# Optimization experiments

Measured on AMD Instinct MI355X. Metric: run time of the kernel, lower is better.

The kernel has to match this reference:

```python
import jax, jax.numpy as jnp
import numpy as np

EPS = 1e-6
EVAL_STEPS = 7
INV_T = 1.0
B, C, H, W = 16, 512, 64, 64
S, R = 1, 64


def setup_inputs() -> dict:
    key = jax.random.key(0)
    kx, kb = jax.random.split(key)
    x = jax.random.uniform(kx, (B, C, H, W), dtype=jnp.float32)
    # bases: F.normalize(rand(S, D, R), dim=1), repeated over batch -> [B*S, D, R]
    D = C // S
    b = jax.random.uniform(kb, (S, D, R), dtype=jnp.float32)
    b = b / jnp.clip(jnp.linalg.norm(b, axis=1, keepdims=True), 1e-12)
    bases = jnp.tile(b, (B, 1, 1))  # [B*S, D, R]
    return {"x": x, "bases": bases}


def _local_step(x, bases, coef):
    # x: [BS, D, N], bases: [BS, D, R], coef: [BS, N, R]
    numer = jnp.einsum('bdn,bdr->bnr', x, bases)
    denom = jnp.einsum('bnr,brk->bnk', coef, jnp.einsum('bdr,bdk->brk', bases, bases))
    coef = coef * numer / (denom + EPS)
    numer = jnp.einsum('bdn,bnr->bdr', x, coef)
    denom = jnp.einsum('bdr,brk->bdk', bases, jnp.einsum('bnr,bnk->brk', coef, coef))
    bases = bases * numer / (denom + EPS)
    return bases, coef


def reference(x, bases):
    batch, channels, height, width = x.shape
    scale = channels // S
    xf = x.reshape(batch * S, scale, height * width)  # [BS, D, N]
    # local_inference (eval mode: eval_steps iterations)
    coef = jnp.einsum('bdn,bdr->bnr', xf, bases)
    coef = jax.nn.softmax(INV_T * coef, axis=-1)
    for _ in range(EVAL_STEPS):
        bases, coef = _local_step(xf, bases, coef)
    # compute_coef: one extra coef update
    numer = jnp.einsum('bdn,bdr->bnr', xf, bases)
    denom = jnp.einsum('bnr,brk->bnk', coef, jnp.einsum('bdr,bdk->brk', bases, bases))
    coef = coef * numer / (denom + EPS)
    out = jnp.einsum('bdr,bnr->bdn', bases, coef)  # bases @ coef^T
    return out.reshape(batch, channels, height, width)
```

## Files before the change

kernel.cpp:

```cpp
#include <hip/hip_runtime.h>
#include <math.h>

#define EPS 1e-6f

constexpr int BSZ = 16;
constexpr int DD  = 512;
constexpr int NN  = 4096;
constexpr int RR  = 64;
constexpr int STEPS = 7;
constexpr int NS_B  = 8;
constexpr int NS_C  = 32;
constexpr int NS_N2 = 8;

typedef _Float16 half_t;
typedef __attribute__((ext_vector_type(8))) _Float16 half8;
typedef __attribute__((ext_vector_type(4))) float f32x4;

__device__ __forceinline__ void fma4s(float4& a, const float4& b, float s) {
  a.x = fmaf(b.x, s, a.x); a.y = fmaf(b.y, s, a.y);
  a.z = fmaf(b.z, s, a.z); a.w = fmaf(b.w, s, a.w);
}
__device__ __forceinline__ void add4(float4& a, const float4& b) {
  a.x += b.x; a.y += b.y; a.z += b.z; a.w += b.w;
}
__device__ __forceinline__ f32x4 mfmah(half8 a, half8 b, f32x4 c) {
  return __builtin_amdgcn_mfma_f32_16x16x32_f16(a, b, c, 0, 0, 0);
}

__device__ __forceinline__ void gload16(const float* g, float* l) {
  __builtin_amdgcn_global_load_lds(
      (const __attribute__((address_space(1))) void*)g,
      (__attribute__((address_space(3))) void*)l, 16, 0, 0);
}

__global__ void __launch_bounds__(256) tcvt16_kernel(const float* __restrict__ src,
                                                     half_t* __restrict__ dh,
                                                     int R, int C) {
  __shared__ float tileT[64 * 65];
  const int b = blockIdx.z, c0 = blockIdx.x << 6, r0 = blockIdx.y << 6;
  const float* sp = src + (long long)b * R * C;
  const int t = threadIdx.x;
  #pragma unroll
  for (int i = 0; i < 4; ++i) {
    const int idx = t + (i << 8);
    const int row = idx >> 4, c4 = (idx & 15) << 2;
    const float4 v = *(const float4*)&sp[(long long)(r0 + row) * C + c0 + c4];
    tileT[(c4 + 0) * 65 + row] = v.x;
    tileT[(c4 + 1) * 65 + row] = v.y;
    tileT[(c4 + 2) * 65 + row] = v.z;
    tileT[(c4 + 3) * 65 + row] = v.w;
  }
  __syncthreads();
  const int orow = t >> 2, och = (t & 3) << 4;
  half8 h0, h1;
  #pragma unroll
  for (int j = 0; j < 8; ++j) h0[j] = (half_t)tileT[orow * 65 + och + j];
  #pragma unroll
  for (int j = 0; j < 8; ++j) h1[j] = (half_t)tileT[orow * 65 + och + 8 + j];
  const long long ob = ((long long)b * C + c0 + orow) * R + r0 + och;
  *(half8*)&dh[ob] = h0;
  *(half8*)&dh[ob + 8] = h1;
}

__global__ void __launch_bounds__(256) cast16_kernel(const float* __restrict__ src,
                                                     half_t* __restrict__ dst,
                                                     long long n) {
  const long long i = ((long long)blockIdx.x * 256 + threadIdx.x) * 8;
  if (i >= n) return;
  const float4 a = *(const float4*)&src[i];
  const float4 c = *(const float4*)&src[i + 4];
  half8 h;
  h[0] = (half_t)a.x; h[1] = (half_t)a.y; h[2] = (half_t)a.z; h[3] = (half_t)a.w;
  h[4] = (half_t)c.x; h[5] = (half_t)c.y; h[6] = (half_t)c.z; h[7] = (half_t)c.w;
  *(half8*)&dst[i] = h;
}

__global__ void __launch_bounds__(256) btb16_kernel(const half_t* __restrict__ BT,
                                                    half_t* __restrict__ Gh) {
  __shared__ float red[64 * 64];
  const int b = blockIdx.x;
  const int t = threadIdx.x;
  const int w = t >> 6;
  const int l = t & 63;
  const int row16 = l & 15;
  const int koff  = (l >> 4) << 3;

  const half_t* ap = BT + ((long long)b * RR + row16) * DD + (w << 7) + koff;

  f32x4 acc[4][4];
  #pragma unroll
  for (int i = 0; i < 4; ++i)
    #pragma unroll
    for (int j = 0; j < 4; ++j) acc[i][j] = (f32x4){0.f, 0.f, 0.f, 0.f};

  #pragma unroll
  for (int kt = 0; kt < 4; ++kt) {
    const int ko = kt << 5;
    half8 af[4];
    #pragma unroll
    for (int rs = 0; rs < 4; ++rs) af[rs] = *(const half8*)&ap[(long long)rs * 16 * DD + ko];
    #pragma unroll
    for (int r1 = 0; r1 < 4; ++r1)
      #pragma unroll
      for (int r2 = 0; r2 < 4; ++r2)
        acc[r1][r2] = mfmah(af[r1], af[r2], acc[r1][r2]);
  }
  for (int ww = 0; ww < 4; ++ww) {
    if (w == ww) {
      #pragma unroll
      for (int r1 = 0; r1 < 4; ++r1)
        #pragma unroll
        for (int r2 = 0; r2 < 4; ++r2)
          #pragma unroll
          for (int j = 0; j < 4; ++j) {
            const int row = (r1 << 4) + ((l >> 4) << 2) + j;
            const int col = (r2 << 4) + row16;
            if (ww == 0) red[row * 64 + col] = acc[r1][r2][j];
            else         red[row * 64 + col] += acc[r1][r2][j];
          }
    }
    __syncthreads();
  }
  for (int i = t; i < 512; i += 256) {
    half8 h;
    #pragma unroll
    for (int j = 0; j < 8; ++j) h[j] = (half_t)red[(i << 3) + j];
    *(half8*)&Gh[(long long)b * 4096 + (i << 3)] = h;
  }
}

template <int MODE>
__global__ void __launch_bounds__(128) fused16_kernel(const half_t* __restrict__ xT,
                                                      const half_t* __restrict__ BT,
                                                      const half_t* __restrict__ Gh,
                                                      float* __restrict__ coef,
                                                      half_t* __restrict__ cbT,
                                                      half_t* __restrict__ cN) {
  __shared__ half_t ctile[(MODE == 1) ? 64 * 40 : 8];
  const int b  = blockIdx.y;
  const int n0 = blockIdx.x << 5;
  const int t  = threadIdx.x;
  const int w  = t >> 6;
  const int l  = t & 63;
  const int row16 = l & 15;
  const int koff  = (l >> 4) << 3;
  const int nrb   = n0 + (w << 4);

  const half_t* ap = xT + ((long long)b * NN + nrb + row16) * DD + koff;
  const half_t* bp = BT + ((long long)b * RR + row16) * DD + koff;

  f32x4 acc[4];
  #pragma unroll
  for (int rs = 0; rs < 4; ++rs) acc[rs] = (f32x4){0.f, 0.f, 0.f, 0.f};

  #pragma unroll
  for (int kt = 0; kt < 16; ++kt) {
    const int ko = kt << 5;
    const half8 av = *(const half8*)&ap[ko];
    #pragma unroll
    for (int rs = 0; rs < 4; ++rs) {
      const half8 bv = *(const half8*)&bp[rs * 16 * DD + ko];
      acc[rs] = mfmah(av, bv, acc[rs]);
    }
  }

  if constexpr (MODE == 0) {
    #pragma unroll
    for (int j = 0; j < 4; ++j) {
      float m = fmaxf(fmaxf(acc[0][j], acc[1][j]), fmaxf(acc[2][j], acc[3][j]));
      m = fmaxf(m, __shfl_xor(m, 1));
      m = fmaxf(m, __shfl_xor(m, 2));
      m = fmaxf(m, __shfl_xor(m, 4));
      m = fmaxf(m, __shfl_xor(m, 8));
      float s = 0.f;
      #pragma unroll
      for (int rs = 0; rs < 4; ++rs) { acc[rs][j] = __expf(acc[rs][j] - m); s += acc[rs][j]; }
      s += __shfl_xor(s, 1); s += __shfl_xor(s, 2);
      s += __shfl_xor(s, 4); s += __shfl_xor(s, 8);
      const float inv = 1.f / s;
      #pragma unroll
      for (int rs = 0; rs < 4; ++rs) acc[rs][j] *= inv;
    }
    #pragma unroll
    for (int rs = 0; rs < 4; ++rs)
      #pragma unroll
      for (int j = 0; j < 4; ++j)
        coef[((long long)b * NN + nrb + ((l >> 4) << 2) + j) * RR + (rs << 4) + row16] = acc[rs][j];
  } else {
    const float* crow = coef + ((long long)b * NN + nrb + row16) * RR;
    const half_t* ghb = Gh + (long long)b * 4096;
    f32x4 dn[4];
    #pragma unroll
    for (int rs = 0; rs < 4; ++rs) dn[rs] = (f32x4){0.f, 0.f, 0.f, 0.f};
    #pragma unroll
    for (int kt = 0; kt < 2; ++kt) {
      const int ko = (kt << 5) + koff;
      const float4 c0 = *(const float4*)&crow[ko];
      const float4 c1 = *(const float4*)&crow[ko + 4];
      half8 ch;
      ch[0] = (half_t)c0.x; ch[1] = (half_t)c0.y; ch[2] = (half_t)c0.z; ch[3] = (half_t)c0.w;
      ch[4] = (half_t)c1.x; ch[5] = (half_t)c1.y; ch[6] = (half_t)c1.z; ch[7] = (half_t)c1.w;
      #pragma unroll
      for (int rs = 0; rs < 4; ++rs) {
        const half8 gh = *(const half8*)&ghb[((rs << 4) + row16) * 64 + ko];
        dn[rs] = mfmah(ch, gh, dn[rs]);
      }
    }
    #pragma unroll
    for (int rs = 0; rs < 4; ++rs)
      #pragma unroll
      for (int j = 0; j < 4; ++j) {
        const int r = (rs << 4) + row16;
        const int nl = ((w << 4) + ((l >> 4) << 2) + j);
        const long long idx = ((long long)b * NN + n0 + nl) * RR + r;
        const float co = coef[idx];
        const float v  = co * acc[rs][j] / (dn[rs][j] + EPS);
        if constexpr (MODE == 1) {
          coef[idx] = v;
          ctile[r * 40 + nl] = (half_t)v;
        } else {
          cN[idx] = (half_t)v;
        }
      }
    if constexpr (MODE == 1) {
      __syncthreads();
      if (t < 64) {
        half_t* dst = cbT + ((long long)b * RR + t) * NN + n0;
        *(half8*)&dst[0]  = *(const half8*)&ctile[t * 40 + 0];
        *(half8*)&dst[8]  = *(const half8*)&ctile[t * 40 + 8];
        *(half8*)&dst[16] = *(const half8*)&ctile[t * 40 + 16];
        *(half8*)&dst[24] = *(const half8*)&ctile[t * 40 + 24];
      }
    }
  }
}

__global__ void __launch_bounds__(128) numer2ctc16_kernel(const half_t* __restrict__ xh,
                                                          const half_t* __restrict__ cbT,
                                                          float* __restrict__ n2p,
                                                          float* __restrict__ ctcp) {
  __shared__ float red[4096];
  const int b = blockIdx.z;
  const int s = blockIdx.y;
  const int t = threadIdx.x;
  const int w = t >> 6;
  const int l = t & 63;
  const int row16 = l & 15;
  const int koff  = (l >> 4) << 3;
  const int nbeg  = s * (NN / NS_N2);

  if (blockIdx.x == DD / 64) {
    const half_t* ap = cbT + ((long long)b * RR + row16) * NN + nbeg + (w << 8) + koff;
    f32x4 acc[4][4];
    #pragma unroll
    for (int i = 0; i < 4; ++i)
      #pragma unroll
      for (int j = 0; j < 4; ++j) acc[i][j] = (f32x4){0.f, 0.f, 0.f, 0.f};
    #pragma unroll
    for (int kt = 0; kt < 8; ++kt) {
      const int ko = kt << 5;
      half8 af[4];
      #pragma unroll
      for (int rs = 0; rs < 4; ++rs) af[rs] = *(const half8*)&ap[(long long)rs * 16 * NN + ko];
      #pragma unroll
      for (int r1 = 0; r1 < 4; ++r1)
        #pragma unroll
        for (int r2 = 0; r2 < 4; ++r2)
          acc[r1][r2] = mfmah(af[r1], af[r2], acc[r1][r2]);
    }
    if (w == 0) {
      #pragma unroll
      for (int r1 = 0; r1 < 4; ++r1)
        #pragma unroll
        for (int r2 = 0; r2 < 4; ++r2)
          #pragma unroll
          for (int j = 0; j < 4; ++j)
            red[((r1 << 4) + ((l >> 4) << 2) + j) * 64 + (r2 << 4) + row16] = acc[r1][r2][j];
    }
    __syncthreads();
    if (w == 1) {
      #pragma unroll
      for (int r1 = 0; r1 < 4; ++r1)
        #pragma unroll
        for (int r2 = 0; r2 < 4; ++r2)
          #pragma unroll
          for (int j = 0; j < 4; ++j)
            red[((r1 << 4) + ((l >> 4) << 2) + j) * 64 + (r2 << 4) + row16] += acc[r1][r2][j];
    }
    __syncthreads();
    float* op = ctcp + ((long long)s * BSZ + b) * 4096;
    for (int i = t; i < 1024; i += 128) ((float4*)op)[i] = ((const float4*)red)[i];
    return;
  }

  const int d0 = blockIdx.x << 6;
  const half_t* ap = xh + ((long long)b * DD + d0 + w * 32 + row16) * NN + nbeg + koff;
  const half_t* cp = cbT + ((long long)b * RR + row16) * NN + nbeg + koff;

  f32x4 acc[2][4];
  #pragma unroll
  for (int ds = 0; ds < 2; ++ds)
    #pragma unroll
    for (int rs = 0; rs < 4; ++rs) acc[ds][rs] = (f32x4){0.f, 0.f, 0.f, 0.f};

  #pragma unroll
  for (int kt = 0; kt < 16; ++kt) {
    const int ko = kt << 5;
    half8 av[2], bf[4];
    #pragma unroll
    for (int ds = 0; ds < 2; ++ds) av[ds] = *(const half8*)&ap[(long long)ds * 16 * NN + ko];
    #pragma unroll
    for (int rs = 0; rs < 4; ++rs) bf[rs] = *(const half8*)&cp[(long long)rs * 16 * NN + ko];
    #pragma unroll
    for (int ds = 0; ds < 2; ++ds)
      #pragma unroll
      for (int rs = 0; rs < 4; ++rs)
        acc[ds][rs] = mfmah(av[ds], bf[rs], acc[ds][rs]);
  }
  float* op = n2p + (((long long)s * BSZ + b) * DD + d0 + w * 32) * RR;
  #pragma unroll
  for (int ds = 0; ds < 2; ++ds)
    #pragma unroll
    for (int rs = 0; rs < 4; ++rs)
      #pragma unroll
      for (int j = 0; j < 4; ++j)
        op[(long long)(ds * 16 + ((l >> 4) << 2) + j) * RR + (rs << 4) + row16] = acc[ds][rs][j];
}

__global__ void __launch_bounds__(256) bupdate16_kernel(float* __restrict__ Bw,
                                                        const float* __restrict__ n2p,
                                                        const float* __restrict__ ctcp,
                                                        half_t* __restrict__ BbT,
                                                        half_t* __restrict__ bD) {
  __shared__ float ct[4096];
  const int b  = blockIdx.y;
  const int d0 = blockIdx.x << 6;
  const int t  = threadIdx.x;
  #pragma unroll
  for (int i = 0; i < 4; ++i) {
    const int w = t + (i << 8);
    float4 s4 = make_float4(0.f, 0.f, 0.f, 0.f);
    #pragma unroll
    for (int sp = 0; sp < NS_N2; ++sp)
      add4(s4, ((const float4*)(ctcp + ((long long)sp * BSZ + b) * 4096))[w]);
    ((float4*)ct)[w] = s4;
  }
  __syncthreads();
  const int dl = t >> 2;
  const int d  = d0 + dl;
  const int rq = (t & 3) << 4;

  float4 ns[4];
  #pragma unroll
  for (int j = 0; j < 4; ++j) ns[j] = make_float4(0.f, 0.f, 0.f, 0.f);
  for (int s = 0; s < NS_N2; ++s) {
    const float4* p = (const float4*)&n2p[(((long long)s * BSZ + b) * DD + d) * RR + rq];
    #pragma unroll
    for (int j = 0; j < 4; ++j) add4(ns[j], p[j]);
  }
  const float4* brow = (const float4*)&Bw[((long long)b * DD + d) * RR];
  float4 dn[4];
  #pragma unroll
  for (int j = 0; j < 4; ++j) dn[j] = make_float4(0.f, 0.f, 0.f, 0.f);
  for (int q = 0; q < 16; ++q) {
    const float4 b4 = brow[q];
    const float4* c0 = (const float4*)&ct[(4 * q + 0) * 64 + rq];
    const float4* c1 = (const float4*)&ct[(4 * q + 1) * 64 + rq];
    const float4* c2 = (const float4*)&ct[(4 * q + 2) * 64 + rq];
    const float4* c3 = (const float4*)&ct[(4 * q + 3) * 64 + rq];
    #pragma unroll
    for (int j = 0; j < 4; ++j) {
      fma4s(dn[j], c0[j], b4.x); fma4s(dn[j], c1[j], b4.y);
      fma4s(dn[j], c2[j], b4.z); fma4s(dn[j], c3[j], b4.w);
    }
  }
  float4* bp = (float4*)&Bw[((long long)b * DD + d) * RR + rq];
  float4 bo[4];
  #pragma unroll
  for (int j = 0; j < 4; ++j) bo[j] = bp[j];
  __syncthreads();
  half_t* tile = (half_t*)ct;
  float4 ov[4];
  #pragma unroll
  for (int j = 0; j < 4; ++j) {
    ov[j].x = bo[j].x * ns[j].x / (dn[j].x + EPS);
    ov[j].y = bo[j].y * ns[j].y / (dn[j].y + EPS);
    ov[j].z = bo[j].z * ns[j].z / (dn[j].z + EPS);
    ov[j].w = bo[j].w * ns[j].w / (dn[j].w + EPS);
    bp[j] = ov[j];
    tile[(rq + (j << 2) + 0) * 64 + dl] = (half_t)ov[j].x;
    tile[(rq + (j << 2) + 1) * 64 + dl] = (half_t)ov[j].y;
    tile[(rq + (j << 2) + 2) * 64 + dl] = (half_t)ov[j].z;
    tile[(rq + (j << 2) + 3) * 64 + dl] = (half_t)ov[j].w;
  }
  if (bD) {
    half_t* dst = bD + ((long long)b * DD + d) * RR + rq;
    half8 h0, h1;
    #pragma unroll
    for (int e = 0; e < 4; ++e) {
      h0[e] = (half_t)ov[0].x, h0[e] = h0[e];
    }
    h0[0] = (half_t)ov[0].x; h0[1] = (half_t)ov[0].y; h0[2] = (half_t)ov[0].z; h0[3] = (half_t)ov[0].w;
    h0[4] = (half_t)ov[1].x; h0[5] = (half_t)ov[1].y; h0[6] = (half_t)ov[1].z; h0[7] = (half_t)ov[1].w;
    h1[0] = (half_t)ov[2].x; h1[1] = (half_t)ov[2].y; h1[2] = (half_t)ov[2].z; h1[3] = (half_t)ov[2].w;
    h1[4] = (half_t)ov[3].x; h1[5] = (half_t)ov[3].y; h1[6] = (half_t)ov[3].z; h1[7] = (half_t)ov[3].w;
    *(half8*)&dst[0] = h0;
    *(half8*)&dst[8] = h1;
  }
  __syncthreads();
  const int r = t >> 2, qc = t & 3;
  half_t* dstT = BbT + ((long long)b * RR + r) * DD + d0 + (qc << 4);
  *(half8*)&dstT[0] = *(const half8*)&tile[r * 64 + (qc << 4)];
  *(half8*)&dstT[8] = *(const half8*)&tile[r * 64 + (qc << 4) + 8];
}

__global__ void __launch_bounds__(256) out16_kernel(const half_t* __restrict__ bD,
                                                    const half_t* __restrict__ cN,
                                                    float* __restrict__ out) {
  __shared__ float ot[16 * 264];
  const int n0 = blockIdx.x << 8;
  const int d0 = blockIdx.y << 4;
  const int b  = blockIdx.z;
  const int t  = threadIdx.x;
  const int w  = t >> 6;
  const int l  = t & 63;
  const int row16 = l & 15;
  const int koff  = (l >> 4) << 3;

  const half_t* ap = bD + ((long long)b * DD + d0 + row16) * RR + koff;
  const half_t* bp = cN + ((long long)b * NN + n0 + (w << 6) + row16) * RR + koff;

  f32x4 acc[4];
  #pragma unroll
  for (int ns = 0; ns < 4; ++ns) acc[ns] = (f32x4){0.f, 0.f, 0.f, 0.f};

  #pragma unroll
  for (int kt = 0; kt < 2; ++kt) {
    const int ko = kt << 5;
    const half8 av = *(const half8*)&ap[ko];
    #pragma unroll
    for (int ns = 0; ns < 4; ++ns) {
      const half8 bv = *(const half8*)&bp[(long long)ns * 16 * RR + ko];
      acc[ns] = mfmah(av, bv, acc[ns]);
    }
  }
  #pragma unroll
  for (int ns = 0; ns < 4; ++ns)
    #pragma unroll
    for (int j = 0; j < 4; ++j)
      ot[(((l >> 4) << 2) + j) * 264 + (w << 6) + (ns << 4) + row16] = acc[ns][j];
  __syncthreads();
  #pragma unroll
  for (int k = 0; k < 4; ++k) {
    const int idx = t + (k << 8);
    const int row = idx >> 6, c4 = (idx & 63) << 2;
    const float4 v = *(const float4*)&ot[row * 264 + c4];
    *(float4*)&out[((long long)b * DD + d0 + row) * NN + n0 + c4] = v;
  }
}


__global__ void __launch_bounds__(256) gram_kernel(const float* __restrict__ M,
                                                   float* __restrict__ outp,
                                                   int rowsPerWave,
                                                   long long batchStride) {
  __shared__ float red[RR * RR];
  const int lane = threadIdx.x & 63;
  const int wid  = threadIdx.x >> 6;
  const int b    = blockIdx.y;
  const long long rowbase = (long long)(blockIdx.x * 4 + wid) * rowsPerWave;
  const float* Mp = M + (long long)b * batchStride + rowbase * RR;
  float acc[RR];
  #pragma unroll
  for (int k = 0; k < RR; ++k) acc[k] = 0.f;
  #pragma unroll 2
  for (int rr = 0; rr < rowsPerWave; ++rr) {
    const float v = Mp[(long long)rr * RR + lane];
    #pragma unroll
    for (int k = 0; k < RR; ++k) acc[k] = fmaf(__shfl(v, k), v, acc[k]);
  }
  for (int w = 0; w < 4; ++w) {
    if (wid == w) {
      if (w == 0) {
        #pragma unroll
        for (int k = 0; k < RR; ++k) red[k * RR + lane] = acc[k];
      } else {
        #pragma unroll
        for (int k = 0; k < RR; ++k) red[k * RR + lane] += acc[k];
      }
    }
    __syncthreads();
  }
  float* op = outp + ((long long)blockIdx.x * BSZ + b) * (RR * RR);
  for (int i = threadIdx.x; i < RR * RR; i += 256) op[i] = red[i];
}

template <int MODE>
__global__ void __launch_bounds__(128) fused_coef_kernel(const float* __restrict__ X,
                                                         const float* __restrict__ Bw,
                                                         const float* __restrict__ btbp,
                                                         float* __restrict__ coef) {
  __shared__ float lds[8192];
  const int b    = blockIdx.y;
  const int n0   = blockIdx.x << 6;
  const int t    = threadIdx.x;
  const int wid  = t >> 6;
  const int lane = t & 63;
  const int rgrp = t & 7;
  const int ngrp = t >> 3;
  const int nl   = ngrp << 2;
  const int r0   = rgrp << 3;
  const float* Xp = X  + (long long)b * DD * NN + n0;
  const float* Bp = Bw + (long long)b * DD * RR;

  float4 acc[4][2];
  #pragma unroll
  for (int i = 0; i < 4; ++i) { acc[i][0] = make_float4(0,0,0,0); acc[i][1] = make_float4(0,0,0,0); }

  auto stage = [&](int buf, int d0) {
    float* xd = lds + (buf << 11);
    float* bd = lds + 4096 + (buf << 11);
    const int rsub = lane >> 4;
    const int c4   = (lane & 15) << 2;
    #pragma unroll
    for (int j = 0; j < 4; ++j) {
      const int q   = (wid << 2) + j;
      const int row = (q << 2) + rsub;
      gload16(&Xp[(long long)(d0 + row) * NN + c4], xd + (q << 8));
      gload16(&Bp[(long long)(d0 + row) * RR + c4], bd + (q << 8));
    }
  };

  stage(0, 0);
  __syncthreads();
  for (int kt = 0; kt < 16; ++kt) {
    const int cur = kt & 1;
    if (kt + 1 < 16) stage(cur ^ 1, (kt + 1) << 5);
    const float* xs = lds + (cur << 11);
    const float* bs = lds + 4096 + (cur << 11);
    #pragma unroll 8
    for (int dd = 0; dd < 32; ++dd) {
      const float4 xv  = *(const float4*)&xs[(dd << 6) + nl];
      const float4 bv0 = *(const float4*)&bs[(dd << 6) + r0];
      const float4 bv1 = *(const float4*)&bs[(dd << 6) + r0 + 4];
      fma4s(acc[0][0], bv0, xv.x); fma4s(acc[0][1], bv1, xv.x);
      fma4s(acc[1][0], bv0, xv.y); fma4s(acc[1][1], bv1, xv.y);
      fma4s(acc[2][0], bv0, xv.z); fma4s(acc[2][1], bv1, xv.z);
      fma4s(acc[3][0], bv0, xv.w); fma4s(acc[3][1], bv1, xv.w);
    }
    __syncthreads();
  }

  if constexpr (MODE == 0) {
    #pragma unroll
    for (int i = 0; i < 4; ++i) {
      float4 a0 = acc[i][0], a1 = acc[i][1];
      float m = fmaxf(fmaxf(fmaxf(a0.x, a0.y), fmaxf(a0.z, a0.w)),
                      fmaxf(fmaxf(a1.x, a1.y), fmaxf(a1.z, a1.w)));
      m = fmaxf(m, __shfl_xor(m, 1));
      m = fmaxf(m, __shfl_xor(m, 2));
      m = fmaxf(m, __shfl_xor(m, 4));
      a0.x = __expf(a0.x - m); a0.y = __expf(a0.y - m);
      a0.z = __expf(a0.z - m); a0.w = __expf(a0.w - m);
      a1.x = __expf(a1.x - m); a1.y = __expf(a1.y - m);
      a1.z = __expf(a1.z - m); a1.w = __expf(a1.w - m);
      float s = a0.x + a0.y + a0.z + a0.w + a1.x + a1.y + a1.z + a1.w;
      s += __shfl_xor(s, 1); s += __shfl_xor(s, 2); s += __shfl_xor(s, 4);
      const float inv = 1.f / s;
      a0.x *= inv; a0.y *= inv; a0.z *= inv; a0.w *= inv;
      a1.x *= inv; a1.y *= inv; a1.z *= inv; a1.w *= inv;
      float* cp = coef + ((long long)b * NN + n0 + nl + i) * RR + r0;
      *(float4*)&cp[0] = a0;
      *(float4*)&cp[4] = a1;
    }
  } else {
    float4* G4  = (float4*)lds;
    float4* CO4 = (float4*)(lds + 4096);
    #pragma unroll
    for (int j = 0; j < 8; ++j) {
      const int wi = t + (j << 7);
      float4 ssum = make_float4(0,0,0,0);
      #pragma unroll
      for (int sp = 0; sp < NS_B; ++sp)
        add4(ssum, ((const float4*)(btbp + ((long long)sp * BSZ + b) * 4096))[wi]);
      G4[wi] = ssum;
    }
    const float4* cof4 = (const float4*)(coef + ((long long)b * NN + n0) * RR);
    #pragma unroll
    for (int j = 0; j < 8; ++j) {
      const int wi = t + (j << 7);
      const int row = wi >> 4, c4 = wi & 15;
      CO4[(row << 4) + (c4 ^ ((row >> 2) & 7))] = cof4[wi];
    }
    __syncthreads();
    const int g = ngrp & 7;
    float4 dn[4][2];
    #pragma unroll
    for (int i = 0; i < 4; ++i) { dn[i][0] = make_float4(0,0,0,0); dn[i][1] = make_float4(0,0,0,0); }
    #pragma unroll 4
    for (int kq = 0; kq < 16; ++kq) {
      float4 g0[4], g1[4];
      #pragma unroll
      for (int jj = 0; jj < 4; ++jj) {
        g0[jj] = G4[(((kq << 2) + jj) << 4) + (rgrp << 1)];
        g1[jj] = G4[(((kq << 2) + jj) << 4) + (rgrp << 1) + 1];
      }
      #pragma unroll
      for (int i = 0; i < 4; ++i) {
        const float4 cv = CO4[((nl + i) << 4) + (kq ^ g)];
        fma4s(dn[i][0], g0[0], cv.x); fma4s(dn[i][1], g1[0], cv.x);
        fma4s(dn[i][0], g0[1], cv.y); fma4s(dn[i][1], g1[1], cv.y);
        fma4s(dn[i][0], g0[2], cv.z); fma4s(dn[i][1], g1[2], cv.z);
        fma4s(dn[i][0], g0[3], cv.w); fma4s(dn[i][1], g1[3], cv.w);
      }
    }
    #pragma unroll
    for (int i = 0; i < 4; ++i) {
      const int row = nl + i;
      const float4 c0 = CO4[(row << 4) + ((rgrp << 1) ^ g)];
      const float4 c1 = CO4[(row << 4) + (((rgrp << 1) + 1) ^ g)];
      float4 o0, o1;
      o0.x = c0.x * acc[i][0].x / (dn[i][0].x + EPS);
      o0.y = c0.y * acc[i][0].y / (dn[i][0].y + EPS);
      o0.z = c0.z * acc[i][0].z / (dn[i][0].z + EPS);
      o0.w = c0.w * acc[i][0].w / (dn[i][0].w + EPS);
      o1.x = c1.x * acc[i][1].x / (dn[i][1].x + EPS);
      o1.y = c1.y * acc[i][1].y / (dn[i][1].y + EPS);
      o1.z = c1.z * acc[i][1].z / (dn[i][1].z + EPS);
      o1.w = c1.w * acc[i][1].w / (dn[i][1].w + EPS);
      float* cp = coef + ((long long)b * NN + n0 + row) * RR + r0;
      *(float4*)&cp[0] = o0;
      *(float4*)&cp[4] = o1;
    }
  }
}

__global__ void __launch_bounds__(128) numer2_kernel(const float* __restrict__ X,
                                                     const float* __restrict__ coef,
                                                     float* __restrict__ n2p) {
  __shared__ float lds[8192];
  const int b    = blockIdx.z;
  const int s    = blockIdx.y;
  const int d0   = blockIdx.x << 6;
  const int t    = threadIdx.x;
  const int wid  = t >> 6;
  const int lane = t & 63;
  const int rgrp = t & 7;
  const int dgrp = t >> 3;
  const int dl   = dgrp << 2;
  const int r0   = rgrp << 3;
  const int nbeg = s * (NN / NS_N2);
  const float* Xp = X + (long long)b * DD * NN + (long long)d0 * NN;
  const float* Cp = coef + (long long)b * NN * RR;

  float4 acc[4][2];
  #pragma unroll
  for (int i = 0; i < 4; ++i) { acc[i][0] = make_float4(0,0,0,0); acc[i][1] = make_float4(0,0,0,0); }

  auto stage = [&](int buf, int nb) {
    float* xd = lds + (buf << 11);
    float* cd = lds + 4096 + (buf << 11);
    {
      const int rsub = lane >> 3, c4 = lane & 7;
      #pragma unroll
      for (int j = 0; j < 4; ++j) {
        const int q   = (wid << 2) + j;
        const int row = (q << 3) + rsub;
        const int sc  = (c4 ^ ((row >> 2) & 7)) << 2;
        gload16(&Xp[(long long)row * NN + nb + sc], xd + (q << 8));
      }
    }
    {
      const int rsub = lane >> 4, c4 = (lane & 15) << 2;
      #pragma unroll
      for (int j = 0; j < 4; ++j) {
        const int q   = (wid << 2) + j;
        const int row = (q << 2) + rsub;
        gload16(&Cp[(long long)(nb + row) * RR + c4], cd + (q << 8));
      }
    }
  };

  stage(0, nbeg);
  __syncthreads();
  const int g = dgrp & 7;
  for (int kt = 0; kt < (NN / NS_N2) / 32; ++kt) {
    const int cur = kt & 1;
    if (kt + 1 < (NN / NS_N2) / 32) stage(cur ^ 1, nbeg + ((kt + 1) << 5));
    const float* xs = lds + (cur << 11);
    const float* cs = lds + 4096 + (cur << 11);
    #pragma unroll 8
    for (int nn = 0; nn < 32; ++nn) {
      const int col = ((((nn >> 2) ^ g) << 2) + (nn & 3));
      float xe[4];
      #pragma unroll
      for (int i = 0; i < 4; ++i) xe[i] = xs[((dl + i) << 5) + col];
      const float4 cv0 = *(const float4*)&cs[(nn << 6) + r0];
      const float4 cv1 = *(const float4*)&cs[(nn << 6) + r0 + 4];
      #pragma unroll
      for (int i = 0; i < 4; ++i) {
        fma4s(acc[i][0], cv0, xe[i]);
        fma4s(acc[i][1], cv1, xe[i]);
      }
    }
    __syncthreads();
  }
  #pragma unroll
  for (int i = 0; i < 4; ++i) {
    float* op = n2p + (((long long)s * BSZ + b) * DD + d0 + dl + i) * RR + r0;
    *(float4*)&op[0] = acc[i][0];
    *(float4*)&op[4] = acc[i][1];
  }
}

__global__ void __launch_bounds__(256) bupdate_fb_kernel(float* __restrict__ Bw,
                                                         const float* __restrict__ n2p,
                                                         const float* __restrict__ ctcp,
                                                         int ns2) {
  __shared__ float ct[4096];
  const int b  = blockIdx.y;
  const int d0 = blockIdx.x << 6;
  #pragma unroll
  for (int i = 0; i < 4; ++i) {
    const int w = threadIdx.x + (i << 8);
    float4 s = make_float4(0.f, 0.f, 0.f, 0.f);
    for (int sp = 0; sp < NS_C; ++sp)
      add4(s, ((const float4*)(ctcp + ((long long)sp * BSZ + b) * 4096))[w]);
    ((float4*)ct)[w] = s;
  }
  __syncthreads();
  const int d  = d0 + (threadIdx.x >> 2);
  const int rq = (threadIdx.x & 3) << 4;

  float4 ns[4];
  #pragma unroll
  for (int j = 0; j < 4; ++j) ns[j] = make_float4(0.f, 0.f, 0.f, 0.f);
  for (int s = 0; s < ns2; ++s) {
    const float4* p = (const float4*)&n2p[(((long long)s * BSZ + b) * DD + d) * RR + rq];
    #pragma unroll
    for (int j = 0; j < 4; ++j) add4(ns[j], p[j]);
  }
  const float4* brow = (const float4*)&Bw[((long long)b * DD + d) * RR];
  float4 dn[4];
  #pragma unroll
  for (int j = 0; j < 4; ++j) dn[j] = make_float4(0.f, 0.f, 0.f, 0.f);
  for (int q = 0; q < 16; ++q) {
    const float4 b4 = brow[q];
    const float4* c0 = (const float4*)&ct[(4 * q + 0) * 64 + rq];
    const float4* c1 = (const float4*)&ct[(4 * q + 1) * 64 + rq];
    const float4* c2 = (const float4*)&ct[(4 * q + 2) * 64 + rq];
    const float4* c3 = (const float4*)&ct[(4 * q + 3) * 64 + rq];
    #pragma unroll
    for (int j = 0; j < 4; ++j) {
      fma4s(dn[j], c0[j], b4.x); fma4s(dn[j], c1[j], b4.y);
      fma4s(dn[j], c2[j], b4.z); fma4s(dn[j], c3[j], b4.w);
    }
  }
  float4* bp = (float4*)&Bw[((long long)b * DD + d) * RR + rq];
  float4 bo[4];
  #pragma unroll
  for (int j = 0; j < 4; ++j) bo[j] = bp[j];
  __syncthreads();
  #pragma unroll
  for (int j = 0; j < 4; ++j) {
    float4 o;
    o.x = bo[j].x * ns[j].x / (dn[j].x + EPS);
    o.y = bo[j].y * ns[j].y / (dn[j].y + EPS);
    o.z = bo[j].z * ns[j].z / (dn[j].z + EPS);
    o.w = bo[j].w * ns[j].w / (dn[j].w + EPS);
    bp[j] = o;
  }
}

__global__ void __launch_bounds__(256) out_kernel(const float* __restrict__ Bw,
                                                  const float* __restrict__ coef,
                                                  float* __restrict__ out) {
  __shared__ float bt [64 * 68];
  __shared__ float ctl[64 * 68];
  const int n0 = blockIdx.x << 6;
  const int d0 = blockIdx.y << 6;
  const int b  = blockIdx.z;
  const int tx = threadIdx.x & 15;
  const int ty = threadIdx.x >> 4;
  for (int t = threadIdx.x; t < 1024; t += 256) {
    const int row = t >> 4, c4 = (t & 15) << 2;
    const float4 v = *(const float4*)&Bw[((long long)b * DD + d0 + row) * RR + c4];
    bt[(c4 + 0) * 68 + row] = v.x; bt[(c4 + 1) * 68 + row] = v.y;
    bt[(c4 + 2) * 68 + row] = v.z; bt[(c4 + 3) * 68 + row] = v.w;
  }
  for (int t = threadIdx.x; t < 1024; t += 256) {
    const int row = t >> 4, c4 = (t & 15) << 2;
    const float4 v = *(const float4*)&coef[((long long)b * NN + n0 + row) * RR + c4];
    ctl[(c4 + 0) * 68 + row] = v.x; ctl[(c4 + 1) * 68 + row] = v.y;
    ctl[(c4 + 2) * 68 + row] = v.z; ctl[(c4 + 3) * 68 + row] = v.w;
  }
  __syncthreads();
  float4 ai[4];
  #pragma unroll
  for (int i = 0; i < 4; ++i) ai[i] = make_float4(0.f, 0.f, 0.f, 0.f);
  #pragma unroll 8
  for (int r = 0; r < 64; ++r) {
    const float4 bv = *(const float4*)&bt [r * 68 + (ty << 2)];
    const float4 cv = *(const float4*)&ctl[r * 68 + (tx << 2)];
    fma4s(ai[0], cv, bv.x); fma4s(ai[1], cv, bv.y);
    fma4s(ai[2], cv, bv.z); fma4s(ai[3], cv, bv.w);
  }
  #pragma unroll
  for (int i = 0; i < 4; ++i)
    *(float4*)&out[((long long)b * DD + d0 + (ty << 2) + i) * NN + n0 + (tx << 2)] = ai[i];
}

extern "C" void kernel_launch(void* const* d_in, const int* in_sizes, int n_in,
                              void* d_out, int out_size, void* d_ws, size_t ws_size,
                              hipStream_t stream) {
  const float* x        = (const float*)d_in[0];
  const float* bases_in = (const float*)d_in[1];
  float* out = (float*)d_out;
  float* ws  = (float*)d_ws;

  float* coef    = ws;
  float* bases_w = coef + (long long)BSZ * NN * RR;
  float* btbp    = bases_w + (long long)BSZ * DD * RR;
  float* ctcp    = btbp + (long long)NS_B * BSZ * 4096;
  float* n2p     = ctcp + (long long)NS_C * BSZ * 4096;
  float* ctcs    = n2p + (long long)NS_N2 * BSZ * DD * RR;
  half_t* xT16   = (half_t*)(ctcs + (long long)BSZ * 4096);
  half_t* xd16   = xT16 + (long long)BSZ * NN * DD;
  half_t* BbT16  = xd16 + (long long)BSZ * NN * DD;
  half_t* cbT16  = BbT16 + (long long)BSZ * RR * DD;
  half_t* Gh16   = cbT16 + (long long)BSZ * RR * NN;
  const long long need = (long long)((char*)(Gh16 + (long long)BSZ * 4096) - (char*)d_ws);

  half_t* cN16 = (half_t*)n2p;
  half_t* bD16 = (half_t*)btbp;

  const dim3 blk256(256);
  const dim3 blk128(128);

  hipMemcpyAsync(bases_w, bases_in, sizeof(float) * BSZ * DD * RR,
                 hipMemcpyDeviceToDevice, stream);

  if ((long long)ws_size >= need) {
    cast16_kernel<<<dim3(16384), blk256, 0, stream>>>(x, xd16, (long long)BSZ * DD * NN);
    tcvt16_kernel<<<dim3(NN / 64, DD / 64, BSZ), blk256, 0, stream>>>(x, xT16, DD, NN);
    tcvt16_kernel<<<dim3(1, DD / 64, BSZ), blk256, 0, stream>>>(bases_w, BbT16, DD, RR);
    fused16_kernel<0><<<dim3(NN / 32, BSZ), blk128, 0, stream>>>(
        xT16, BbT16, nullptr, coef, nullptr, nullptr);

    for (int it = 0; it < STEPS; ++it) {
      btb16_kernel<<<dim3(BSZ), blk256, 0, stream>>>(BbT16, Gh16);
      fused16_kernel<1><<<dim3(NN / 32, BSZ), blk128, 0, stream>>>(
          xT16, BbT16, Gh16, coef, cbT16, nullptr);
      numer2ctc16_kernel<<<dim3(DD / 64 + 1, NS_N2, BSZ), blk128, 0, stream>>>(
          xd16, cbT16, n2p, ctcp);
      bupdate16_kernel<<<dim3(DD / 64, BSZ), blk256, 0, stream>>>(
          bases_w, n2p, ctcp, BbT16, (it == STEPS - 1) ? bD16 : nullptr);
    }
    btb16_kernel<<<dim3(BSZ), blk256, 0, stream>>>(BbT16, Gh16);
    fused16_kernel<2><<<dim3(NN / 32, BSZ), blk128, 0, stream>>>(
        xT16, BbT16, Gh16, coef, nullptr, cN16);
    out16_kernel<<<dim3(NN / 256, DD / 16, BSZ), blk256, 0, stream>>>(bD16, cN16, out);
  } else {
    fused_coef_kernel<0><<<dim3(NN / 64, BSZ), blk128, 0, stream>>>(x, bases_w, nullptr, coef);
    for (int it = 0; it < STEPS; ++it) {
      gram_kernel<<<dim3(NS_B, BSZ), blk256, 0, stream>>>(bases_w, btbp, DD / (NS_B * 4),
                                                          (long long)DD * RR);
      fused_coef_kernel<1><<<dim3(NN / 64, BSZ), blk128, 0, stream>>>(x, bases_w, btbp, coef);
      gram_kernel<<<dim3(NS_C, BSZ), blk256, 0, stream>>>(coef, ctcp, NN / (NS_C * 4),
                                                          (long long)NN * RR);
      numer2_kernel<<<dim3(DD / 64, NS_N2, BSZ), blk128, 0, stream>>>(x, coef, n2p);
      bupdate_fb_kernel<<<dim3(DD / 64, BSZ), blk256, 0, stream>>>(bases_w, n2p, ctcp, NS_N2);
    }
    gram_kernel<<<dim3(NS_B, BSZ), blk256, 0, stream>>>(bases_w, btbp, DD / (NS_B * 4),
                                                        (long long)DD * RR);
    fused_coef_kernel<1><<<dim3(NN / 64, BSZ), blk128, 0, stream>>>(x, bases_w, btbp, coef);
    out_kernel<<<dim3(NN / 64, DD / 64, BSZ), blk256, 0, stream>>>(bases_w, coef, out);
  }
}
```

Baseline: 923.5 us.

## Fuse x conversions into one pass and fold bases Gram into bases update

Merges the two fp16 conversions of x (plain cast and transpose) into one kernel that reads x once and writes both layouts. Removes the per-iteration btb16 launch by computing each 64-row slice's partial B^T B inside bupdate16 with MFMA and atomically accumulating into an fp32 Gram buffer, which numer2ctc16 zeroes beforehand. The fused coefficient kernel now reads the fp32 Gram and converts it to half on the fly. This trades launches and one full pass over x for fp32 atomics and some extra fp32 loads.

New measurement: 880.7 us. 1.05x faster.

```diff
diff --git a/kernel.cpp b/kernel.cpp
--- a/kernel.cpp
+++ b/kernel.cpp
@@ -14,6 +14,7 @@
 
 typedef _Float16 half_t;
 typedef __attribute__((ext_vector_type(8))) _Float16 half8;
+typedef __attribute__((ext_vector_type(4))) _Float16 half4v;
 typedef __attribute__((ext_vector_type(4))) float f32x4;
 
 __device__ __forceinline__ void fma4s(float4& a, const float4& b, float s) {
@@ -31,6 +32,38 @@
   __builtin_amdgcn_global_load_lds(
       (const __attribute__((address_space(1))) void*)g,
       (__attribute__((address_space(3))) void*)l, 16, 0, 0);
+}
+
+__global__ void __launch_bounds__(256) xcvt16_kernel(const float* __restrict__ src,
+                                                     half_t* __restrict__ xd,
+                                                     half_t* __restrict__ xT) {
+  __shared__ float tileT[64 * 65];
+  const int b = blockIdx.z, c0 = blockIdx.x << 6, r0 = blockIdx.y << 6;
+  const float* sp = src + (long long)b * DD * NN;
+  const int t = threadIdx.x;
+  #pragma unroll
+  for (int i = 0; i < 4; ++i) {
+    const int idx = t + (i << 8);
+    const int row = idx >> 4, c4 = (idx & 15) << 2;
+    const float4 v = *(const float4*)&sp[(long long)(r0 + row) * NN + c0 + c4];
+    half4v h;
+    h[0] = (half_t)v.x; h[1] = (half_t)v.y; h[2] = (half_t)v.z; h[3] = (half_t)v.w;
+    *(half4v*)&xd[((long long)b * DD + r0 + row) * NN + c0 + c4] = h;
+    tileT[(c4 + 0) * 65 + row] = v.x;
+    tileT[(c4 + 1) * 65 + row] = v.y;
+    tileT[(c4 + 2) * 65 + row] = v.z;
+    tileT[(c4 + 3) * 65 + row] = v.w;
+  }
+  __syncthreads();
+  const int orow = t >> 2, och = (t & 3) << 4;
+  half8 h0, h1;
+  #pragma unroll
+  for (int j = 0; j < 8; ++j) h0[j] = (half_t)tileT[orow * 65 + och + j];
+  #pragma unroll
+  for (int j = 0; j < 8; ++j) h1[j] = (half_t)tileT[orow * 65 + och + 8 + j];
+  const long long ob = ((long long)b * NN + c0 + orow) * DD + r0 + och;
+  *(half8*)&xT[ob] = h0;
+  *(half8*)&xT[ob + 8] = h1;
 }
 
 __global__ void __launch_bounds__(256) tcvt16_kernel(const float* __restrict__ src,
@@ -62,21 +95,8 @@
   *(half8*)&dh[ob + 8] = h1;
 }
 
-__global__ void __launch_bounds__(256) cast16_kernel(const float* __restrict__ src,
-                                                     half_t* __restrict__ dst,
-                                                     long long n) {
-  const long long i = ((long long)blockIdx.x * 256 + threadIdx.x) * 8;
-  if (i >= n) return;
-  const float4 a = *(const float4*)&src[i];
-  const float4 c = *(const float4*)&src[i + 4];
-  half8 h;
-  h[0] = (half_t)a.x; h[1] = (half_t)a.y; h[2] = (half_t)a.z; h[3] = (half_t)a.w;
-  h[4] = (half_t)c.x; h[5] = (half_t)c.y; h[6] = (half_t)c.z; h[7] = (half_t)c.w;
-  *(half8*)&dst[i] = h;
-}
-
 __global__ void __launch_bounds__(256) btb16_kernel(const half_t* __restrict__ BT,
-                                                    half_t* __restrict__ Gh) {
+                                                    float* __restrict__ Gf) {
   __shared__ float red[64 * 64];
   const int b = blockIdx.x;
   const int t = threadIdx.x;
@@ -121,18 +141,14 @@
     }
     __syncthreads();
   }
-  for (int i = t; i < 512; i += 256) {
-    half8 h;
-    #pragma unroll
-    for (int j = 0; j < 8; ++j) h[j] = (half_t)red[(i << 3) + j];
-    *(half8*)&Gh[(long long)b * 4096 + (i << 3)] = h;
-  }
+  float* op = Gf + (long long)b * 4096;
+  for (int i = t; i < 1024; i += 256) ((float4*)op)[i] = ((const float4*)red)[i];
 }
 
 template <int MODE>
 __global__ void __launch_bounds__(128) fused16_kernel(const half_t* __restrict__ xT,
                                                       const half_t* __restrict__ BT,
-                                                      const half_t* __restrict__ Gh,
+                                                      const float* __restrict__ Gf,
                                                       float* __restrict__ coef,
                                                       half_t* __restrict__ cbT,
                                                       half_t* __restrict__ cN) {
@@ -188,7 +204,7 @@
         coef[((long long)b * NN + nrb + ((l >> 4) << 2) + j) * RR + (rs << 4) + row16] = acc[rs][j];
   } else {
     const float* crow = coef + ((long long)b * NN + nrb + row16) * RR;
-    const half_t* ghb = Gh + (long long)b * 4096;
+    const float* gfb  = Gf + (long long)b * 4096;
     f32x4 dn[4];
     #pragma unroll
     for (int rs = 0; rs < 4; ++rs) dn[rs] = (f32x4){0.f, 0.f, 0.f, 0.f};
@@ -202,7 +218,11 @@
       ch[4] = (half_t)c1.x; ch[5] = (half_t)c1.y; ch[6] = (half_t)c1.z; ch[7] = (half_t)c1.w;
       #pragma unroll
       for (int rs = 0; rs < 4; ++rs) {
-        const half8 gh = *(const half8*)&ghb[((rs << 4) + row16) * 64 + ko];
+        const float4 g0 = *(const float4*)&gfb[((rs << 4) + row16) * 64 + ko];
+        const float4 g1 = *(const float4*)&gfb[((rs << 4) + row16) * 64 + ko + 4];
+        half8 gh;
+        gh[0] = (half_t)g0.x; gh[1] = (half_t)g0.y; gh[2] = (half_t)g0.z; gh[3] = (half_t)g0.w;
+        gh[4] = (half_t)g1.x; gh[5] = (half_t)g1.y; gh[6] = (half_t)g1.z; gh[7] = (half_t)g1.w;
         dn[rs] = mfmah(ch, gh, dn[rs]);
       }
     }
@@ -238,7 +258,8 @@
 __global__ void __launch_bounds__(128) numer2ctc16_kernel(const half_t* __restrict__ xh,
                                                           const half_t* __restrict__ cbT,
                                                           float* __restrict__ n2p,
-                                                          float* __restrict__ ctcp) {
+                                                          float* __restrict__ ctcp,
+                                                          float* __restrict__ Gf) {
   __shared__ float red[4096];
   const int b = blockIdx.z;
   const int s = blockIdx.y;
@@ -250,6 +271,7 @@
   const int nbeg  = s * (NN / NS_N2);
 
   if (blockIdx.x == DD / 64) {
+    ((float4*)(Gf + (long long)b * 4096 + (s << 9)))[t] = make_float4(0.f, 0.f, 0.f, 0.f);
     const half_t* ap = cbT + ((long long)b * RR + row16) * NN + nbeg + (w << 8) + koff;
     f32x4 acc[4][4];
     #pragma unroll
@@ -331,8 +353,9 @@
                                                         const float* __restrict__ n2p,
                                                         const float* __restrict__ ctcp,
                                                         half_t* __restrict__ BbT,
+                                                        float* __restrict__ Gf,
                                                         half_t* __restrict__ bD) {
-  __shared__ float ct[4096];
+  __shared__ __align__(16) float ct[4096];
   const int b  = blockIdx.y;
   const int d0 = blockIdx.x << 6;
   const int t  = threadIdx.x;
@@ -388,18 +411,14 @@
     ov[j].z = bo[j].z * ns[j].z / (dn[j].z + EPS);
     ov[j].w = bo[j].w * ns[j].w / (dn[j].w + EPS);
     bp[j] = ov[j];
-    tile[(rq + (j << 2) + 0) * 64 + dl] = (half_t)ov[j].x;
-    tile[(rq + (j << 2) + 1) * 64 + dl] = (half_t)ov[j].y;
-    tile[(rq + (j << 2) + 2) * 64 + dl] = (half_t)ov[j].z;
-    tile[(rq + (j << 2) + 3) * 64 + dl] = (half_t)ov[j].w;
+    tile[(rq + (j << 2) + 0) * 72 + dl] = (half_t)ov[j].x;
+    tile[(rq + (j << 2) + 1) * 72 + dl] = (half_t)ov[j].y;
+    tile[(rq + (j << 2) + 2) * 72 + dl] = (half_t)ov[j].z;
+    tile[(rq + (j << 2) + 3) * 72 + dl] = (half_t)ov[j].w;
   }
   if (bD) {
     half_t* dst = bD + ((long long)b * DD + d) * RR + rq;
     half8 h0, h1;
-    #pragma unroll
-    for (int e = 0; e < 4; ++e) {
-      h0[e] = (half_t)ov[0].x, h0[e] = h0[e];
-    }
     h0[0] = (half_t)ov[0].x; h0[1] = (half_t)ov[0].y; h0[2] = (half_t)ov[0].z; h0[3] = (half_t)ov[0].w;
     h0[4] = (half_t)ov[1].x; h0[5] = (half_t)ov[1].y; h0[6] = (half_t)ov[1].z; h0[7] = (half_t)ov[1].w;
     h1[0] = (half_t)ov[2].x; h1[1] = (half_t)ov[2].y; h1[2] = (half_t)ov[2].z; h1[3] = (half_t)ov[2].w;
@@ -408,10 +427,36 @@
     *(half8*)&dst[8] = h1;
   }
   __syncthreads();
+  {
+    const int wv = t >> 6;
+    const int l  = t & 63;
+    const int row16 = l & 15;
+    const int koff2 = (l >> 4) << 3;
+    const half_t* a1 = tile + ((wv << 4) + row16) * 72 + koff2;
+    f32x4 g[4];
+    #pragma unroll
+    for (int rs = 0; rs < 4; ++rs) g[rs] = (f32x4){0.f, 0.f, 0.f, 0.f};
+    #pragma unroll
+    for (int kt = 0; kt < 2; ++kt) {
+      const int ko = kt << 5;
+      const half8 av = *(const half8*)&a1[ko];
+      #pragma unroll
+      for (int rs = 0; rs < 4; ++rs) {
+        const half8 bv = *(const half8*)&tile[((rs << 4) + row16) * 72 + koff2 + ko];
+        g[rs] = mfmah(av, bv, g[rs]);
+      }
+    }
+    float* gfb = Gf + (long long)b * 4096;
+    #pragma unroll
+    for (int rs = 0; rs < 4; ++rs)
+      #pragma unroll
+      for (int j = 0; j < 4; ++j)
+        atomicAdd(&gfb[((wv << 4) + ((l >> 4) << 2) + j) * 64 + (rs << 4) + row16], g[rs][j]);
+  }
   const int r = t >> 2, qc = t & 3;
   half_t* dstT = BbT + ((long long)b * RR + r) * DD + d0 + (qc << 4);
-  *(half8*)&dstT[0] = *(const half8*)&tile[r * 64 + (qc << 4)];
-  *(half8*)&dstT[8] = *(const half8*)&tile[r * 64 + (qc << 4) + 8];
+  *(half8*)&dstT[0] = *(const half8*)&tile[r * 72 + (qc << 4)];
+  *(half8*)&dstT[8] = *(const half8*)&tile[r * 72 + (qc << 4) + 8];
 }
 
 __global__ void __launch_bounds__(256) out16_kernel(const half_t* __restrict__ bD,
@@ -823,8 +868,8 @@
   float* btbp    = bases_w + (long long)BSZ * DD * RR;
   float* ctcp    = btbp + (long long)NS_B * BSZ * 4096;
   float* n2p     = ctcp + (long long)NS_C * BSZ * 4096;
-  float* ctcs    = n2p + (long long)NS_N2 * BSZ * DD * RR;
-  half_t* xT16   = (half_t*)(ctcs + (long long)BSZ * 4096);
+  float* Gf      = n2p + (long long)NS_N2 * BSZ * DD * RR;
+  half_t* xT16   = (half_t*)(Gf + (long long)BSZ * 4096);
   half_t* xd16   = xT16 + (long long)BSZ * NN * DD;
   half_t* BbT16  = xd16 + (long long)BSZ * NN * DD;
   half_t* cbT16  = BbT16 + (long long)BSZ * RR * DD;
@@ -841,24 +886,22 @@
                  hipMemcpyDeviceToDevice, stream);
 
   if ((long long)ws_size >= need) {
-    cast16_kernel<<<dim3(16384), blk256, 0, stream>>>(x, xd16, (long long)BSZ * DD * NN);
-    tcvt16_kernel<<<dim3(NN / 64, DD / 64, BSZ), blk256, 0, stream>>>(x, xT16, DD, NN);
+    xcvt16_kernel<<<dim3(NN / 64, DD / 64, BSZ), blk256, 0, stream>>>(x, xd16, xT16);
     tcvt16_kernel<<<dim3(1, DD / 64, BSZ), blk256, 0, stream>>>(bases_w, BbT16, DD, RR);
+    btb16_kernel<<<dim3(BSZ), blk256, 0, stream>>>(BbT16, Gf);
     fused16_kernel<0><<<dim3(NN / 32, BSZ), blk128, 0, stream>>>(
         xT16, BbT16, nullptr, coef, nullptr, nullptr);
 
     for (int it = 0; it < STEPS; ++it) {
-      btb16_kernel<<<dim3(BSZ), blk256, 0, stream>>>(BbT16, Gh16);
       fused16_kernel<1><<<dim3(NN / 32, BSZ), blk128, 0, stream>>>(
-          xT16, BbT16, Gh16, coef, cbT16, nullptr);
+          xT16, BbT16, Gf, coef, cbT16, nullptr);
       numer2ctc16_kernel<<<dim3(DD / 64 + 1, NS_N2, BSZ), blk128, 0, stream>>>(
-          xd16, cbT16, n2p, ctcp);
+          xd16, cbT16, n2p, ctcp, Gf);
       bupdate16_kernel<<<dim3(DD / 64, BSZ), blk256, 0, stream>>>(
-          bases_w, n2p, ctcp, BbT16, (it == STEPS - 1) ? bD16 : nullptr);
-    }
-    btb16_kernel<<<dim3(BSZ), blk256, 0, stream>>>(BbT16, Gh16);
+          bases_w, n2p, ctcp, BbT16, Gf, (it == STEPS - 1) ? bD16 : nullptr);
+    }
     fused16_kernel<2><<<dim3(NN / 32, BSZ), blk128, 0, stream>>>(
-        xT16, BbT16, Gh16, coef, nullptr, cN16);
+        xT16, BbT16, Gf, coef, nullptr, cN16);
     out16_kernel<<<dim3(NN / 256, DD / 16, BSZ), blk256, 0, stream>>>(bD16, cN16, out);
   } else {
     fused_coef_kernel<0><<<dim3(NN / 64, BSZ), blk128, 0, stream>>>(x, bases_w, nullptr, coef);
```
